# Kernel tuning notes

Hardware: AMD Instinct MI355X
Metric: run time of the kernel (lower is better)

The kernel has to match this reference:

```python
import jax, jax.numpy as jnp
import numpy as np

B, L, H, N = 32, 4096, 256, 512
THR = 0.0          # sim_threshold
NEG = -1e9         # mask value for softmax
SLOPE = 0.2        # LeakyReLU negative slope
EPS = 1e-8         # torch cosine_similarity eps


def _span_mean(cs, st, ed):
    # cs: [B, L+1, H] inclusive prefix sums with leading zero row
    hi = jnp.take_along_axis(cs, (ed + 1)[:, :, None], axis=1)  # [B,N,H]
    lo = jnp.take_along_axis(cs, st[:, :, None], axis=1)
    cnt = (ed - st + 1).astype(cs.dtype)[:, :, None]
    return (hi - lo) / cnt


def _leaky(x):
    return jnp.where(x >= 0, x, SLOPE * x)


def _forward(embeddings, W_trip, b_trip, edge_emb, W_attn, b_attn, W_gat, b_gat,
             asp_st, asp_len, opi_st, opi_len, sent_id):
    Bv, Lv, Hv = embeddings.shape
    asp_ed = asp_st + asp_len  # [B,N], always < L by construction
    opi_ed = opi_st + opi_len

    # span means via prefix sums (replaces per-triplet slice .mean(0))
    cs = jnp.concatenate([jnp.zeros((Bv, 1, Hv), embeddings.dtype),
                          jnp.cumsum(embeddings, axis=1)], axis=1)  # [B,L+1,H]
    asp_repr = _span_mean(cs, asp_st, asp_ed)  # [B,N,H]
    opi_repr = _span_mean(cs, opi_st, opi_ed)
    sent_vec = jax.nn.one_hot(sent_id, 3, dtype=embeddings.dtype)  # [B,N,3]

    node_in = jnp.concatenate([asp_repr, opi_repr, sent_vec], axis=-1)  # [B,N,2H+3]
    node = node_in @ W_trip + b_trip  # [B,N,H] triplet_proj

    # pairwise cosine similarity (torch eps semantics)
    nrm = jnp.sqrt(jnp.sum(node * node, axis=-1))  # [B,N]
    dots = jnp.einsum('bih,bjh->bij', node, node)
    sim = dots / jnp.maximum(nrm[:, :, None] * nrm[:, None, :], EPS)  # [B,N,N]

    eye = jnp.eye(N, dtype=bool)[None]
    same_asp = (asp_st[:, :, None] == asp_st[:, None, :]) & (asp_ed[:, :, None] == asp_ed[:, None, :])
    same_opi = (opi_st[:, :, None] == opi_st[:, None, :]) & (opi_ed[:, :, None] == opi_ed[:, None, :])
    pass_sim = (sim > THR) & ~eye
    mask0 = pass_sim & same_asp  # edge (src=i, tgt=j), type 0
    mask1 = pass_sim & same_opi  # type 1
    # em[b, tgt, src, type]
    em = jnp.stack([jnp.swapaxes(mask0, 1, 2), jnp.swapaxes(mask1, 1, 2)], axis=-1)

    # attn_fc(leaky_relu(concat[node_tgt, node_src, edge_emb])) decomposes linearly
    lnode = _leaky(node)            # [B,N,H]
    ledge = _leaky(edge_emb)        # [2,H]
    a_tgt = (lnode @ W_attn[:H]).squeeze(-1)        # [B,N]
    a_src = (lnode @ W_attn[H:2 * H]).squeeze(-1)   # [B,N]
    a_e = (ledge @ W_attn[2 * H:]).squeeze(-1)      # [2]
    score = (a_tgt[:, :, None, None] + a_src[:, None, :, None]
             + a_e[None, None, None, :] + b_attn[0])  # [B,N,N,2]

    masked = jnp.where(em, score, NEG)
    w = jax.nn.softmax(masked.reshape(Bv, N, -1), axis=-1).reshape(Bv, N, N, 2)
    w = w * em.astype(w.dtype)  # exact zeros on non-edges / neighborless rows

    # aggregate msgs = concat[node_src, edge_emb[type]]
    w_node = w.sum(-1)                                   # [B,tgt,src]
    agg_node = jnp.einsum('bki,bih->bkh', w_node, node)  # [B,N,H]
    agg_e = w.sum(2) @ edge_emb                          # [B,N,H]
    agg = jnp.concatenate([agg_node, agg_e], axis=-1)    # [B,N,2H]
    upd = jax.nn.relu(agg @ W_gat + b_gat)               # gat_proj + relu

    has_neigh = em.any(axis=(2, 3))                      # [B,N]
    node_out = jnp.where(has_neigh[:, :, None], upd, node)

    # original skips the whole batch element if it has no edges at all
    b_has_edge = em.any(axis=(1, 2, 3))                  # [B]
    node_add = jnp.where(b_has_edge[:, None, None], node_out, 0.0)

    center = (asp_st + opi_st) // 2                      # [B,N], < L
    b_idx = jnp.broadcast_to(jnp.arange(Bv)[:, None], center.shape)
    enhanced = embeddings.at[b_idx, center].add(node_add)
    return enhanced


def setup_inputs() -> dict:
    key = jax.random.key(0)
    ks = jax.random.split(key, 12)
    embeddings = jax.random.normal(ks[0], (B, L, H), jnp.float32)
    W_trip = jax.random.normal(ks[1], (2 * H + 3, H), jnp.float32) * 0.05
    b_trip = jnp.zeros((H,), jnp.float32)
    edge_emb = jax.random.normal(ks[2], (2, H), jnp.float32) * 0.05
    W_attn = jax.random.normal(ks[3], (3 * H, 1), jnp.float32) * 0.05
    b_attn = jnp.zeros((1,), jnp.float32)
    W_gat = jax.random.normal(ks[4], (2 * H, H), jnp.float32) * 0.05
    b_gat = jnp.zeros((H,), jnp.float32)
    asp_st = jax.random.randint(ks[5], (B, N), 0, 128, dtype=jnp.int32)
    asp_len = jax.random.randint(ks[6], (B, N), 0, 8, dtype=jnp.int32)
    opi_st = jax.random.randint(ks[7], (B, N), 0, 128, dtype=jnp.int32)
    opi_len = jax.random.randint(ks[8], (B, N), 0, 8, dtype=jnp.int32)
    sent_id = jax.random.randint(ks[9], (B, N), 0, 3, dtype=jnp.int32)
    return dict(embeddings=embeddings, W_trip=W_trip, b_trip=b_trip, edge_emb=edge_emb,
                W_attn=W_attn, b_attn=b_attn, W_gat=W_gat, b_gat=b_gat,
                asp_st=asp_st, asp_len=asp_len, opi_st=opi_st, opi_len=opi_len,
                sent_id=sent_id)


def reference(embeddings, W_trip, b_trip, edge_emb, W_attn, b_attn, W_gat, b_gat,
              asp_st, asp_len, opi_st, opi_len, sent_id):
    return _forward(embeddings, W_trip, b_trip, edge_emb, W_attn, b_attn, W_gat, b_gat,
                    asp_st, asp_len, opi_st, opi_len, sent_id)
```

## Files before the change

### kernel.cpp

```cpp
#include <hip/hip_runtime.h>
#include <math.h>

#define Bn 32
#define Ln 4096
#define ROWS 16384
#define LR 136
#define SLOPEC 0.2f
#define NEGSENT -1e30f

typedef __attribute__((ext_vector_type(4))) float f32x4;
typedef __attribute__((ext_vector_type(4))) unsigned short u16x4;

__device__ __forceinline__ void copy_lin(const float* __restrict__ emb,
        float* __restrict__ out, long start, int count, int tid) {
    const f32x4* s4 = (const f32x4*)emb;
    f32x4* d4 = (f32x4*)out;
    for (int i = tid; i < count; i += 256)
        d4[start + i] = s4[start + i];
}

__device__ __forceinline__ f32x4 leaky4(f32x4 v) {
    f32x4 r;
    r.x = v.x >= 0.f ? v.x : SLOPEC * v.x;
    r.y = v.y >= 0.f ? v.y : SLOPEC * v.y;
    r.z = v.z >= 0.f ? v.z : SLOPEC * v.z;
    r.w = v.w >= 0.f ? v.w : SLOPEC * v.w;
    return r;
}

__device__ __forceinline__ f32x4 bf4_to_f32(u16x4 h) {
    union { unsigned int u; float f; } t;
    f32x4 r;
    t.u = (unsigned)h.x << 16; r.x = t.f;
    t.u = (unsigned)h.y << 16; r.y = t.f;
    t.u = (unsigned)h.z << 16; r.z = t.f;
    t.u = (unsigned)h.w << 16; r.w = t.f;
    return r;
}

__device__ __forceinline__ unsigned short f_to_bf16(float f) {
    union { float f; unsigned int u; } t;
    t.f = f;
    unsigned int u = t.u;
    u += 0x7FFFu + ((u >> 16) & 1u);
    return (unsigned short)(u >> 16);
}

__global__ __launch_bounds__(256) void k_pre(const float* __restrict__ Wtrip,
        const float* __restrict__ btrip, const float* __restrict__ Eemb,
        const float* __restrict__ Wattn, const float* __restrict__ Wgat,
        const int* __restrict__ ast, const int* __restrict__ alen,
        const int* __restrict__ ost, const int* __restrict__ olen,
        const float* __restrict__ emb, float* __restrict__ out,
        float* __restrict__ WtG, float* __restrict__ W3g, float* __restrict__ btg,
        float* __restrict__ ae, float* __restrict__ ve,
        int* __restrict__ keys, int* __restrict__ bflag) {
    int bid = blockIdx.x, tid = threadIdx.x;
    copy_lin(emb, out, (long)bid * 2048, 2048, tid);
    __shared__ float Als[32][68];
    __shared__ float Bls[32][64];
    __shared__ float red[4];
    __shared__ float vr0[8][32], vr1[8][32];
    if (bid < 32) {
        int mat = bid >> 4, t = bid & 15;
        int m0 = (t >> 2) << 6, n0 = (t & 3) << 6;
        const float* A = Wtrip + mat * 65536;
        int r0 = (tid & 15) << 2, c0 = (tid >> 4) << 2;
        float acc[4][4] = {};
        for (int kk = 0; kk < 256; kk += 32) {
            __syncthreads();
            #pragma unroll
            for (int p = 0; p < 2; ++p) {
                int idx = tid + (p << 8);
                int row = idx >> 3, kq = (idx & 7) << 2;
                const float4 v = *(const float4*)(A + (size_t)(m0 + row) * 256 + kk + kq);
                Als[kq + 0][row] = v.x; Als[kq + 1][row] = v.y;
                Als[kq + 2][row] = v.z; Als[kq + 3][row] = v.w;
            }
            #pragma unroll
            for (int p = 0; p < 2; ++p) {
                int idx = tid + (p << 8);
                int k = idx >> 4, hq = (idx & 15) << 2;
                *(float4*)(&Bls[k][hq]) = *(const float4*)(Wgat + (size_t)(kk + k) * 256 + n0 + hq);
            }
            __syncthreads();
            #pragma unroll
            for (int k = 0; k < 32; ++k) {
                float4 a  = *(const float4*)(&Als[k][r0]);
                float4 bv = *(const float4*)(&Bls[k][c0]);
                acc[0][0] += a.x*bv.x; acc[0][1] += a.x*bv.y; acc[0][2] += a.x*bv.z; acc[0][3] += a.x*bv.w;
                acc[1][0] += a.y*bv.x; acc[1][1] += a.y*bv.y; acc[1][2] += a.y*bv.z; acc[1][3] += a.y*bv.w;
                acc[2][0] += a.z*bv.x; acc[2][1] += a.z*bv.y; acc[2][2] += a.z*bv.z; acc[2][3] += a.z*bv.w;
                acc[3][0] += a.w*bv.x; acc[3][1] += a.w*bv.y; acc[3][2] += a.w*bv.z; acc[3][3] += a.w*bv.w;
            }
        }
        #pragma unroll
        for (int i = 0; i < 4; ++i)
            #pragma unroll
            for (int j = 0; j < 4; ++j)
                WtG[mat * 65536 + (size_t)(m0 + r0 + i) * 256 + n0 + c0 + j] = acc[i][j];
    } else if (bid == 32) {
        float s = 0.f;
        for (int k = 0; k < 256; ++k) s += btrip[k] * Wgat[(size_t)k * 256 + tid];
        btg[tid] = s;
    } else if (bid == 33) {
        if (tid < Bn) bflag[tid] = 0;
        #pragma unroll
        for (int e = 0; e < 2; ++e) {
            float x = Eemb[e * 256 + tid];
            float lx = x >= 0.f ? x : SLOPEC * x;
            float s = lx * Wattn[512 + tid];
            #pragma unroll
            for (int o = 32; o; o >>= 1) s += __shfl_down(s, o);
            if ((tid & 63) == 0) red[tid >> 6] = s;
            __syncthreads();
            if (tid == 0) ae[e] = red[0] + red[1] + red[2] + red[3];
            __syncthreads();
        }
    } else if (bid < 37) {
        int s = bid - 34;
        float acc = 0.f;
        for (int k = 0; k < 256; ++k)
            acc += Wtrip[(size_t)(512 + s) * 256 + k] * Wgat[(size_t)k * 256 + tid];
        W3g[s * 256 + tid] = acc;
    } else if (bid < 45) {
        int j = bid - 37;
        int n0 = j << 5;
        int nl = tid & 31, kg = tid >> 5;
        float p0 = 0.f, p1 = 0.f;
        for (int kk = 0; kk < 32; ++kk) {
            int k = (kg << 5) + kk;
            float w = Wgat[(size_t)(256 + k) * 256 + n0 + nl];
            p0 += Eemb[k] * w;
            p1 += Eemb[256 + k] * w;
        }
        vr0[kg][nl] = p0; vr1[kg][nl] = p1;
        __syncthreads();
        if (tid < 32) {
            float s0 = 0.f, s1 = 0.f;
            #pragma unroll
            for (int g = 0; g < 8; ++g) { s0 += vr0[g][tid]; s1 += vr1[g][tid]; }
            ve[n0 + tid] = s0;
            ve[256 + n0 + tid] = s1;
        }
    } else if (bid < 109) {
        int row = (bid - 45) * 256 + tid;
        keys[row] = (((ast[row] << 3) | alen[row]) << 10) | ((ost[row] << 3) | olen[row]);
    }
}

__global__ __launch_bounds__(256) void k_pq(const float* __restrict__ emb,
        const float* __restrict__ Wtrip, const float* __restrict__ WtG,
        float* __restrict__ PQf, unsigned short* __restrict__ PQh,
        float* __restrict__ out) {
    __shared__ float Als[32][68];
    __shared__ float Bls[32][64];
    int tid = threadIdx.x;
    {
        int bid = blockIdx.y * 68 + blockIdx.x;
        copy_lin(emb, out, 2097152L + (long)bid * 1024, 1024, tid);
    }
    int m0 = blockIdx.x << 6;
    int j = blockIdx.y;
    const float* Bp;
    if (j < 4)       Bp = Wtrip + (j << 6);
    else if (j < 8)  Bp = Wtrip + 65536 + ((j - 4) << 6);
    else if (j < 12) Bp = WtG + ((j - 8) << 6);
    else             Bp = WtG + 65536 + ((j - 12) << 6);
    int r0 = (tid & 15) << 2;
    int c0 = (tid >> 4) << 2;
    float acc[4][4] = {};
    for (int kk = 0; kk < 256; kk += 32) {
        __syncthreads();
        #pragma unroll
        for (int p = 0; p < 2; ++p) {
            int idx = tid + (p << 8);
            int row = idx >> 3;
            int kq = (idx & 7) << 2;
            int m = m0 + row;
            int b = m / LR;
            int l = m - b * LR;
            const float4 v = *(const float4*)(emb + (size_t)(b * Ln + l) * 256 + kk + kq);
            Als[kq + 0][row] = v.x; Als[kq + 1][row] = v.y;
            Als[kq + 2][row] = v.z; Als[kq + 3][row] = v.w;
        }
        #pragma unroll
        for (int p = 0; p < 2; ++p) {
            int idx = tid + (p << 8);
            int k = idx >> 4;
            int hq = (idx & 15) << 2;
            *(float4*)(&Bls[k][hq]) = *(const float4*)(Bp + (size_t)(kk + k) * 256 + hq);
        }
        __syncthreads();
        #pragma unroll
        for (int k = 0; k < 32; ++k) {
            float4 a  = *(const float4*)(&Als[k][r0]);
            float4 bv = *(const float4*)(&Bls[k][c0]);
            acc[0][0] += a.x*bv.x; acc[0][1] += a.x*bv.y; acc[0][2] += a.x*bv.z; acc[0][3] += a.x*bv.w;
            acc[1][0] += a.y*bv.x; acc[1][1] += a.y*bv.y; acc[1][2] += a.y*bv.z; acc[1][3] += a.y*bv.w;
            acc[2][0] += a.z*bv.x; acc[2][1] += a.z*bv.y; acc[2][2] += a.z*bv.z; acc[2][3] += a.z*bv.w;
            acc[3][0] += a.w*bv.x; acc[3][1] += a.w*bv.y; acc[3][2] += a.w*bv.z; acc[3][3] += a.w*bv.w;
        }
    }
    if (j < 8) {
        #pragma unroll
        for (int i = 0; i < 4; ++i)
            #pragma unroll
            for (int jj = 0; jj < 4; ++jj)
                PQf[(size_t)(m0 + r0 + i) * 512 + (j << 6) + c0 + jj] = acc[i][jj];
    } else {
        #pragma unroll
        for (int i = 0; i < 4; ++i)
            #pragma unroll
            for (int jj = 0; jj < 4; ++jj)
                PQh[(size_t)(m0 + r0 + i) * 512 + ((j - 8) << 6) + c0 + jj] =
                    f_to_bf16(acc[i][jj]);
    }
}

__global__ __launch_bounds__(256) void k_combine(const float* __restrict__ PQf,
        const unsigned short* __restrict__ PQh,
        const float* __restrict__ Wtrip, const float* __restrict__ btrip,
        const int* __restrict__ sid,
        const int* __restrict__ ast, const int* __restrict__ alen,
        const int* __restrict__ ost, const int* __restrict__ olen,
        const float* __restrict__ Wattn, const float* __restrict__ W3g,
        const float* __restrict__ btg, const float* __restrict__ emb,
        float* __restrict__ out, float* __restrict__ node,
        unsigned short* __restrict__ nodeWh,
        float* __restrict__ atg, float* __restrict__ asr) {
    int bid = blockIdx.x, tid = threadIdx.x;
    int wv = tid >> 6, lane = tid & 63;
    copy_lin(emb, out, 3211264L + (long)bid * 768, 768, tid);

    int s = ((bid & 7) << 9) | (bid >> 3);
    int row = (s << 2) + wv;
    int b = row >> 9;
    int as_ = ast[row], al = alen[row];
    int os_ = ost[row], ol = olen[row];
    int c = lane << 2;
    const float* Pb = PQf + (size_t)b * LR * 512 + c;
    const unsigned short* Ph = PQh + (size_t)b * LR * 512 + c;

    f32x4 asum = {0.f,0.f,0.f,0.f}, osum = asum, p2 = asum, q2 = asum;
    for (int i = 0; i <= al; ++i) {
        size_t off = (size_t)(as_ + i) * 512;
        asum += *(const f32x4*)(Pb + off);
        p2   += bf4_to_f32(*(const u16x4*)(Ph + off));
    }
    for (int i = 0; i <= ol; ++i) {
        size_t off = (size_t)(os_ + i) * 512 + 256;
        osum += *(const f32x4*)(Pb + off);
        q2   += bf4_to_f32(*(const u16x4*)(Ph + off));
    }
    float ra = 1.f / (float)(al + 1), ro = 1.f / (float)(ol + 1);
    int sd = sid[row];

    f32x4 x = asum * ra + osum * ro
            + *(const f32x4*)(Wtrip + (size_t)(512 + sd) * 256 + c)
            + *(const f32x4*)(btrip + c);
    *(f32x4*)(node + (size_t)row * 256 + c) = x;

    f32x4 nw = p2 * ra + q2 * ro
             + *(const f32x4*)(W3g + sd * 256 + c)
             + *(const f32x4*)(btg + c);
    u16x4 nwh;
    nwh.x = f_to_bf16(nw.x); nwh.y = f_to_bf16(nw.y);
    nwh.z = f_to_bf16(nw.z); nwh.w = f_to_bf16(nw.w);
    *(u16x4*)(nodeWh + (size_t)row * 256 + c) = nwh;

    f32x4 lx = leaky4(x);
    f32x4 w1 = *(const f32x4*)(Wattn + c);
    f32x4 w2 = *(const f32x4*)(Wattn + 256 + c);
    float s1 = lx.x*w1.x + lx.y*w1.y + lx.z*w1.z + lx.w*w1.w;
    float s2 = lx.x*w2.x + lx.y*w2.y + lx.z*w2.z + lx.w*w2.w;
    #pragma unroll
    for (int o = 32; o; o >>= 1) {
        s1 += __shfl_xor(s1, o);
        s2 += __shfl_xor(s2, o);
    }
    if (lane == 0) { atg[row] = s1; asr[row] = s2; }
}

__global__ __launch_bounds__(256) void k_edges(
        const float* __restrict__ node, const unsigned short* __restrict__ nodeWh,
        const float* __restrict__ atg, const float* __restrict__ asr,
        const float* __restrict__ ae, const float* __restrict__ battn,
        const float* __restrict__ ve, const float* __restrict__ bgat,
        const int* __restrict__ keys,
        const float* __restrict__ emb, float* __restrict__ out,
        float* __restrict__ nadd, int* __restrict__ bflag) {
    int bid = blockIdx.x;
    int tid = threadIdx.x;
    int wv = tid >> 6, lane = tid & 63;

    copy_lin(emb, out, 6356992L + (long)bid * 496, 496, tid);

    int s = ((bid & 7) << 9) | (bid >> 3);
    int tgt = (s << 2) + wv;
    int b = tgt >> 9, base = b << 9, lt = tgt & 511;

    int mykey = keys[tgt];
    int ka = mykey >> 10, ko = mykey & 1023;

    unsigned long long mA[8], mO[8];
    #pragma unroll
    for (int j = 0; j < 8; ++j) {
        int ls = (j << 6) + lane;
        int k2 = keys[base + ls];
        bool self = (ls == lt);
        mA[j] = __ballot(((k2 >> 10) == ka) && !self);
        mO[j] = __ballot(((k2 & 1023) == ko) && !self);
    }

    f32x4 xt4 = *(const f32x4*)(node + (size_t)tgt * 256 + (lane << 2));
    float a_t = atg[tgt];
    float ae0 = ae[0], ae1 = ae[1], b0 = battn[0];

    float s0a[8], s1a[8];
    unsigned long long mK[8];
    #pragma unroll
    for (int j = 0; j < 8; ++j) {
        s0a[j] = NEGSENT; s1a[j] = NEGSENT;
        unsigned long long m = mA[j] | mO[j];
        while (m) {
            int bit = __builtin_ctzll(m); m &= m - 1;
            int gs = base + (j << 6) + bit;
            f32x4 y = *(const f32x4*)(node + (size_t)gs * 256 + (lane << 2));
            float p = xt4.x * y.x + xt4.y * y.y + xt4.z * y.z + xt4.w * y.w;
            #pragma unroll
            for (int o = 32; o; o >>= 1) p += __shfl_xor(p, o);
            if (p > 0.f && lane == bit) {
                float bs = a_t + asr[gs] + b0;
                if ((mA[j] >> bit) & 1) s0a[j] = bs + ae0;
                if ((mO[j] >> bit) & 1) s1a[j] = bs + ae1;
            }
        }
        mK[j] = __ballot(s0a[j] > -1e29f || s1a[j] > -1e29f);
    }

    float mx = NEGSENT;
    #pragma unroll
    for (int j = 0; j < 8; ++j) mx = fmaxf(mx, fmaxf(s0a[j], s1a[j]));
    #pragma unroll
    for (int o = 32; o; o >>= 1) mx = fmaxf(mx, __shfl_xor(mx, o));
    bool has = mx > -1e29f;

    float se0 = 0.f, se1 = 0.f;
    #pragma unroll
    for (int j = 0; j < 8; ++j) {
        se0 += expf(s0a[j] - mx);
        se1 += expf(s1a[j] - mx);
    }
    #pragma unroll
    for (int o = 32; o; o >>= 1) { se0 += __shfl_xor(se0, o); se1 += __shfl_xor(se1, o); }
    float rden = 1.f / (se0 + se1);

    f32x4 res;
    if (has) {
        f32x4 agg4 = {0.f, 0.f, 0.f, 0.f};
        #pragma unroll
        for (int j = 0; j < 8; ++j) {
            unsigned long long m = mK[j];
            while (m) {
                int bit = __builtin_ctzll(m); m &= m - 1;
                int gs = base + (j << 6) + bit;
                float w0 = __shfl(s0a[j], bit);
                float w1 = __shfl(s1a[j], bit);
                float wt = (expf(w0 - mx) + expf(w1 - mx)) * rden;
                f32x4 nw = bf4_to_f32(*(const u16x4*)(nodeWh + (size_t)gs * 256 + (lane << 2)));
                agg4.x += wt * nw.x; agg4.y += wt * nw.y;
                agg4.z += wt * nw.z; agg4.w += wt * nw.w;
            }
        }
        f32x4 v1 = *(const f32x4*)(ve + (lane << 2));
        f32x4 v2 = *(const f32x4*)(ve + 256 + (lane << 2));
        f32x4 bg = *(const f32x4*)(bgat + (lane << 2));
        float c0 = se0 * rden, c1 = se1 * rden;
        res.x = fmaxf(agg4.x + c0 * v1.x + c1 * v2.x + bg.x, 0.f);
        res.y = fmaxf(agg4.y + c0 * v1.y + c1 * v2.y + bg.y, 0.f);
        res.z = fmaxf(agg4.z + c0 * v1.z + c1 * v2.z + bg.z, 0.f);
        res.w = fmaxf(agg4.w + c0 * v1.w + c1 * v2.w + bg.w, 0.f);
        if (lane == 0) bflag[b] = 1;
    } else {
        res = xt4;
    }
    *(f32x4*)(nadd + (size_t)tgt * 256 + (lane << 2)) = res;
}

__global__ __launch_bounds__(256) void k_scatter(const float* __restrict__ emb,
        const float* __restrict__ nadd,
        const int* __restrict__ ast, const int* __restrict__ ost,
        const int* __restrict__ bflag, float* __restrict__ out) {
    int b = blockIdx.x >> 7;
    int r = blockIdx.x & 127;
    int tid = threadIdx.x;

    __shared__ int cen[512];
    __shared__ unsigned long long s_mask[8];
    for (int n = tid; n < 512; n += 256)
        cen[n] = (ast[(b << 9) + n] + ost[(b << 9) + n]) >> 1;
    __syncthreads();
    #pragma unroll
    for (int p = 0; p < 2; ++p) {
        int n = tid + (p << 8);
        unsigned long long bal = __ballot(cen[n] == r);
        if ((tid & 63) == 0) s_mask[(p << 2) + (tid >> 6)] = bal;
    }
    __syncthreads();
    size_t o = ((size_t)b * Ln + r) * 256 + tid;
    float acc = emb[o];
    if (bflag[b]) {
        for (int w = 0; w < 8; ++w) {
            unsigned long long m = s_mask[w];
            while (m) {
                int n = (w << 6) + __builtin_ctzll(m); m &= m - 1;
                acc += nadd[((size_t)(b << 9) + n) * 256 + tid];
            }
        }
    }
    out[o] = acc;
}

extern "C" void kernel_launch(void* const* d_in, const int* in_sizes, int n_in,
                              void* d_out, int out_size, void* d_ws, size_t ws_size,
                              hipStream_t stream) {
    const float* emb   = (const float*)d_in[0];
    const float* Wtrip = (const float*)d_in[1];
    const float* btrip = (const float*)d_in[2];
    const float* Eemb  = (const float*)d_in[3];
    const float* Wattn = (const float*)d_in[4];
    const float* battn = (const float*)d_in[5];
    const float* Wgat  = (const float*)d_in[6];
    const float* bgat  = (const float*)d_in[7];
    const int* ast  = (const int*)d_in[8];
    const int* alen = (const int*)d_in[9];
    const int* ost  = (const int*)d_in[10];
    const int* olen = (const int*)d_in[11];
    const int* sid  = (const int*)d_in[12];
    float* out = (float*)d_out;

    float* ws    = (float*)d_ws;
    float* PQf   = ws;
    float* node  = PQf + (size_t)4352 * 512;
    float* nadd  = node + (size_t)ROWS * 256;
    float* WtG   = nadd + (size_t)ROWS * 256;
    float* W3g   = WtG + 2 * 65536;
    float* btg   = W3g + 768;
    float* atg   = btg + 256;
    float* asr   = atg + ROWS;
    float* ae    = asr + ROWS;
    float* ve    = ae + 2;
    int* bflag   = (int*)(ve + 512);
    int* keys    = bflag + Bn;
    unsigned short* PQh    = (unsigned short*)(keys + ROWS + 32);
    unsigned short* nodeWh = PQh + (size_t)4352 * 512;

    k_pre<<<1024, 256, 0, stream>>>(Wtrip, btrip, Eemb, Wattn, Wgat,
                                    ast, alen, ost, olen, emb, out,
                                    WtG, W3g, btg, ae, ve, keys, bflag);
    k_pq<<<dim3(68, 16), 256, 0, stream>>>(emb, Wtrip, WtG, PQf, PQh, out);
    k_combine<<<ROWS / 4, 256, 0, stream>>>(PQf, PQh, Wtrip, btrip, sid,
                                            ast, alen, ost, olen,
                                            Wattn, W3g, btg, emb, out, node, nodeWh,
                                            atg, asr);
    k_edges<<<ROWS / 4, 256, 0, stream>>>(node, nodeWh, atg, asr, ae, battn, ve, bgat,
                                          keys, emb, out, nadd, bflag);
    k_scatter<<<Bn * 128, 256, 0, stream>>>(emb, nadd, ast, ost, bflag, out);
}
```

Measured before the change: 142.2 us.

## Compute the WtG half of the PQ GEMM with bf16 MFMA

```diff
diff --git a/kernel.cpp b/kernel.cpp
--- a/kernel.cpp
+++ b/kernel.cpp
@@ -10,6 +10,7 @@
 
 typedef __attribute__((ext_vector_type(4))) float f32x4;
 typedef __attribute__((ext_vector_type(4))) unsigned short u16x4;
+typedef __attribute__((ext_vector_type(8))) short bf16x8;
 
 __device__ __forceinline__ void copy_lin(const float* __restrict__ emb,
         float* __restrict__ out, long start, int count, int tid) {
@@ -52,7 +53,8 @@
         const int* __restrict__ ast, const int* __restrict__ alen,
         const int* __restrict__ ost, const int* __restrict__ olen,
         const float* __restrict__ emb, float* __restrict__ out,
-        float* __restrict__ WtG, float* __restrict__ W3g, float* __restrict__ btg,
+        unsigned short* __restrict__ WtGT, unsigned short* __restrict__ embh,
+        float* __restrict__ W3g, float* __restrict__ btg,
         float* __restrict__ ae, float* __restrict__ ve,
         int* __restrict__ keys, int* __restrict__ bflag) {
     int bid = blockIdx.x, tid = threadIdx.x;
@@ -98,7 +100,8 @@
         for (int i = 0; i < 4; ++i)
             #pragma unroll
             for (int j = 0; j < 4; ++j)
-                WtG[mat * 65536 + (size_t)(m0 + r0 + i) * 256 + n0 + c0 + j] = acc[i][j];
+                WtGT[(size_t)(mat * 256 + n0 + c0 + j) * 256 + m0 + r0 + i] =
+                    f_to_bf16(acc[i][j]);
     } else if (bid == 32) {
         float s = 0.f;
         for (int k = 0; k < 256; ++k) s += btrip[k] * Wgat[(size_t)k * 256 + tid];
@@ -146,11 +149,21 @@
     } else if (bid < 109) {
         int row = (bid - 45) * 256 + tid;
         keys[row] = (((ast[row] << 3) | alen[row]) << 10) | ((ost[row] << 3) | olen[row]);
+    } else if (bid < 381) {
+        int rbase = (bid - 109) << 4;
+        #pragma unroll
+        for (int i = 0; i < 16; ++i) {
+            int row = rbase + i;
+            int b2 = row / LR, l2 = row - b2 * LR;
+            embh[(size_t)row * 256 + tid] =
+                f_to_bf16(emb[((size_t)b2 * Ln + l2) * 256 + tid]);
+        }
     }
 }
 
 __global__ __launch_bounds__(256) void k_pq(const float* __restrict__ emb,
-        const float* __restrict__ Wtrip, const float* __restrict__ WtG,
+        const float* __restrict__ Wtrip,
+        const unsigned short* __restrict__ embh, const unsigned short* __restrict__ WtGT,
         float* __restrict__ PQf, unsigned short* __restrict__ PQh,
         float* __restrict__ out) {
     __shared__ float Als[32][68];
@@ -162,59 +175,72 @@
     }
     int m0 = blockIdx.x << 6;
     int j = blockIdx.y;
-    const float* Bp;
-    if (j < 4)       Bp = Wtrip + (j << 6);
-    else if (j < 8)  Bp = Wtrip + 65536 + ((j - 4) << 6);
-    else if (j < 12) Bp = WtG + ((j - 8) << 6);
-    else             Bp = WtG + 65536 + ((j - 12) << 6);
-    int r0 = (tid & 15) << 2;
-    int c0 = (tid >> 4) << 2;
-    float acc[4][4] = {};
-    for (int kk = 0; kk < 256; kk += 32) {
-        __syncthreads();
-        #pragma unroll
-        for (int p = 0; p < 2; ++p) {
-            int idx = tid + (p << 8);
-            int row = idx >> 3;
-            int kq = (idx & 7) << 2;
-            int m = m0 + row;
-            int b = m / LR;
-            int l = m - b * LR;
-            const float4 v = *(const float4*)(emb + (size_t)(b * Ln + l) * 256 + kk + kq);
-            Als[kq + 0][row] = v.x; Als[kq + 1][row] = v.y;
-            Als[kq + 2][row] = v.z; Als[kq + 3][row] = v.w;
-        }
-        #pragma unroll
-        for (int p = 0; p < 2; ++p) {
-            int idx = tid + (p << 8);
-            int k = idx >> 4;
-            int hq = (idx & 15) << 2;
-            *(float4*)(&Bls[k][hq]) = *(const float4*)(Bp + (size_t)(kk + k) * 256 + hq);
-        }
-        __syncthreads();
-        #pragma unroll
-        for (int k = 0; k < 32; ++k) {
-            float4 a  = *(const float4*)(&Als[k][r0]);
-            float4 bv = *(const float4*)(&Bls[k][c0]);
-            acc[0][0] += a.x*bv.x; acc[0][1] += a.x*bv.y; acc[0][2] += a.x*bv.z; acc[0][3] += a.x*bv.w;
-            acc[1][0] += a.y*bv.x; acc[1][1] += a.y*bv.y; acc[1][2] += a.y*bv.z; acc[1][3] += a.y*bv.w;
-            acc[2][0] += a.z*bv.x; acc[2][1] += a.z*bv.y; acc[2][2] += a.z*bv.z; acc[2][3] += a.z*bv.w;
-            acc[3][0] += a.w*bv.x; acc[3][1] += a.w*bv.y; acc[3][2] += a.w*bv.z; acc[3][3] += a.w*bv.w;
-        }
-    }
+
     if (j < 8) {
+        const float* Bp = Wtrip + ((j < 4) ? (j << 6) : (65536 + ((j - 4) << 6)));
+        int r0 = (tid & 15) << 2;
+        int c0 = (tid >> 4) << 2;
+        float acc[4][4] = {};
+        for (int kk = 0; kk < 256; kk += 32) {
+            __syncthreads();
+            #pragma unroll
+            for (int p = 0; p < 2; ++p) {
+                int idx = tid + (p << 8);
+                int row = idx >> 3;
+                int kq = (idx & 7) << 2;
+                int m = m0 + row;
+                int b = m / LR;
+                int l = m - b * LR;
+                const float4 v = *(const float4*)(emb + (size_t)(b * Ln + l) * 256 + kk + kq);
+                Als[kq + 0][row] = v.x; Als[kq + 1][row] = v.y;
+                Als[kq + 2][row] = v.z; Als[kq + 3][row] = v.w;
+            }
+            #pragma unroll
+            for (int p = 0; p < 2; ++p) {
+                int idx = tid + (p << 8);
+                int k = idx >> 4;
+                int hq = (idx & 15) << 2;
+                *(float4*)(&Bls[k][hq]) = *(const float4*)(Bp + (size_t)(kk + k) * 256 + hq);
+            }
+            __syncthreads();
+            #pragma unroll
+            for (int k = 0; k < 32; ++k) {
+                float4 a  = *(const float4*)(&Als[k][r0]);
+                float4 bv = *(const float4*)(&Bls[k][c0]);
+                acc[0][0] += a.x*bv.x; acc[0][1] += a.x*bv.y; acc[0][2] += a.x*bv.z; acc[0][3] += a.x*bv.w;
+                acc[1][0] += a.y*bv.x; acc[1][1] += a.y*bv.y; acc[1][2] += a.y*bv.z; acc[1][3] += a.y*bv.w;
+                acc[2][0] += a.z*bv.x; acc[2][1] += a.z*bv.y; acc[2][2] += a.z*bv.z; acc[2][3] += a.z*bv.w;
+                acc[3][0] += a.w*bv.x; acc[3][1] += a.w*bv.y; acc[3][2] += a.w*bv.z; acc[3][3] += a.w*bv.w;
+            }
+        }
         #pragma unroll
         for (int i = 0; i < 4; ++i)
             #pragma unroll
             for (int jj = 0; jj < 4; ++jj)
                 PQf[(size_t)(m0 + r0 + i) * 512 + (j << 6) + c0 + jj] = acc[i][jj];
     } else {
-        #pragma unroll
-        for (int i = 0; i < 4; ++i)
-            #pragma unroll
-            for (int jj = 0; jj < 4; ++jj)
-                PQh[(size_t)(m0 + r0 + i) * 512 + ((j - 8) << 6) + c0 + jj] =
-                    f_to_bf16(acc[i][jj]);
+        int jn = j - 8;
+        int wv = tid >> 6, lane = tid & 63;
+        int m0w = m0 + (wv << 4);
+        int n0 = jn << 6;
+        int fr = lane & 15;
+        int kq = (lane >> 4) << 3;
+        f32x4 acc2[4] = {};
+        for (int k0 = 0; k0 < 256; k0 += 32) {
+            bf16x8 a = *(const bf16x8*)(embh + (size_t)(m0w + fr) * 256 + k0 + kq);
+            #pragma unroll
+            for (int nf = 0; nf < 4; ++nf) {
+                bf16x8 bfr = *(const bf16x8*)(WtGT + (size_t)(n0 + (nf << 4) + fr) * 256 + k0 + kq);
+                acc2[nf] = __builtin_amdgcn_mfma_f32_16x16x32_bf16(a, bfr, acc2[nf], 0, 0, 0);
+            }
+        }
+        int r0w = (lane >> 4) << 2;
+        #pragma unroll
+        for (int nf = 0; nf < 4; ++nf)
+            #pragma unroll
+            for (int r = 0; r < 4; ++r)
+                PQh[(size_t)(m0w + r0w + r) * 512 + n0 + (nf << 4) + fr] =
+                    f_to_bf16(acc2[nf][r]);
     }
 }
 
@@ -444,8 +470,7 @@
     float* PQf   = ws;
     float* node  = PQf + (size_t)4352 * 512;
     float* nadd  = node + (size_t)ROWS * 256;
-    float* WtG   = nadd + (size_t)ROWS * 256;
-    float* W3g   = WtG + 2 * 65536;
+    float* W3g   = nadd + (size_t)ROWS * 256;
     float* btg   = W3g + 768;
     float* atg   = btg + 256;
     float* asr   = atg + ROWS;
@@ -455,11 +480,13 @@
     int* keys    = bflag + Bn;
     unsigned short* PQh    = (unsigned short*)(keys + ROWS + 32);
     unsigned short* nodeWh = PQh + (size_t)4352 * 512;
+    unsigned short* embh   = nodeWh + (size_t)ROWS * 256;
+    unsigned short* WtGT   = embh + (size_t)4352 * 256;
 
     k_pre<<<1024, 256, 0, stream>>>(Wtrip, btrip, Eemb, Wattn, Wgat,
                                     ast, alen, ost, olen, emb, out,
-                                    WtG, W3g, btg, ae, ve, keys, bflag);
-    k_pq<<<dim3(68, 16), 256, 0, stream>>>(emb, Wtrip, WtG, PQf, PQh, out);
+                                    WtGT, embh, W3g, btg, ae, ve, keys, bflag);
+    k_pq<<<dim3(68, 16), 256, 0, stream>>>(emb, Wtrip, embh, WtGT, PQf, PQh, out);
     k_combine<<<ROWS / 4, 256, 0, stream>>>(PQf, PQh, Wtrip, btrip, sid,
                                             ast, alen, ost, olen,
                                             Wattn, W3g, btg, emb, out, node, nodeWh,
```

Measured after the change: 131.4 us. 7.6% less time.
